# Kernel tuning notes

Measured on AMD Instinct MI355X. Metric: run time of the kernel, lower is better.

## Reference

```python
import jax, jax.numpy as jnp
import numpy as np

TEMPERATURE = 0.1
NORM_EPS = 1e-12          # F.normalize default eps
SMALL_VAL = float(np.finfo(np.float32).tiny)  # pytorch-metric-learning small_val(float32)
NEG_INF = float(np.finfo(np.float32).min)     # c_f.neg_inf for masked logsumexp


def setup_inputs() -> dict:
    key = jax.random.key(0)
    k1, k2 = jax.random.split(key)
    N, D = 8192, 128
    emb = jax.random.normal(k1, (N, D), dtype=jnp.float32)
    labels = jax.random.randint(k2, (N,), 0, 1000, dtype=jnp.int64)
    return {"emb": emb, "labels": labels}


def reference(emb, labels):
    N = emb.shape[0]
    # F.normalize(emb, dim=1): x / max(||x||, eps)
    norms = jnp.linalg.norm(emb, axis=1, keepdims=True)
    x = emb / jnp.maximum(norms, NORM_EPS)

    # cosine similarity matrix [N, N], scaled by temperature
    mat = jnp.matmul(x, x.T) / TEMPERATURE

    same = labels[:, None] == labels[None, :]
    diag = jnp.eye(N, dtype=bool)
    pos_mask = same & ~diag          # same label, i != j
    keep_mask = ~diag                # pos + neg (all off-diagonal)

    # numerical stability: subtract detached row max (over full row, incl. diagonal)
    mat_max = jax.lax.stop_gradient(jnp.max(mat, axis=1, keepdims=True))
    mat = mat - mat_max

    # masked logsumexp over off-diagonal entries
    masked = jnp.where(keep_mask, mat, NEG_INF)
    denom = jax.nn.logsumexp(masked, axis=1, keepdims=True)  # [N, 1]

    log_prob = mat - denom
    pos_f = pos_mask.astype(mat.dtype)
    mean_log_prob_pos = jnp.sum(pos_f * log_prob, axis=1) / (
        jnp.sum(pos_f, axis=1) + SMALL_VAL
    )
    losses = -mean_log_prob_pos  # per-element losses
    # SumReducer: sum over elements
    return jnp.sum(losses)
```

## Files before the change

### kernel.cpp

```cpp
#include <hip/hip_runtime.h>
#include <hip/hip_bf16.h>


typedef __bf16 bf16_t;
typedef __bf16 bf16x2 __attribute__((ext_vector_type(2)));
typedef __bf16 bf16x8 __attribute__((ext_vector_type(8)));
typedef float f32x16 __attribute__((ext_vector_type(16)));

#define NN 8192
#define DIM 128
#define NCLASS 1024
#define MAIN_BLOCKS 2080
#define SMALL_VAL 1.17549435e-38f
#define L2E10 14.4269504089f
#define LN2 0.69314718056f


__global__ __launch_bounds__(256) void normalize_kernel(const float* __restrict__ emb,
                                                        bf16_t* __restrict__ xsw,
                                                        bf16_t* __restrict__ xrow,
                                                        float* __restrict__ se_acc,
                                                        float* __restrict__ out) {
    int row  = blockIdx.x * 4 + (threadIdx.x >> 6);
    int lane = threadIdx.x & 63;
    float2 v = ((const float2*)emb)[row * 64 + lane];
    float ss = v.x * v.x + v.y * v.y;
#pragma unroll
    for (int m = 1; m < 64; m <<= 1) ss += __shfl_xor(ss, m, 64);
    float inv = 1.0f / fmaxf(sqrtf(ss), 1e-12f);
    bf16x2 o; o.x = (bf16_t)(v.x * inv); o.y = (bf16_t)(v.y * inv);
    int f = lane >> 3, hh = (lane >> 2) & 1, j = (lane & 3) << 1;
    *(bf16x2*)(xsw + ((size_t)(row >> 5) * 4096) + f * 512 + hh * 256 + (row & 31) * 8 + j) = o;
    *(bf16x2*)(xrow + (size_t)row * DIM + 2 * lane) = o;
    if (threadIdx.x < 4) se_acc[blockIdx.x * 4 + threadIdx.x] = 0.f;
    if (blockIdx.x == 0 && threadIdx.x == 0) *out = 0.f;
}

__global__ __launch_bounds__(256) void csum_kernel(const bf16_t* __restrict__ xrow,
                                                   const int* __restrict__ labels,
                                                   float* __restrict__ csum,
                                                   int* __restrict__ hist) {
    __shared__ float cs[DIM];
    __shared__ int cw[4];
    int cls = blockIdx.x;
    int wv = threadIdx.x >> 6, lane = threadIdx.x & 63;
    if (threadIdx.x < DIM) cs[threadIdx.x] = 0.f;
    __syncthreads();
    float s0 = 0.f, s1 = 0.f;
    int cnt = 0;
    const int4* lab4 = (const int4*)(labels + wv * 2048);
    for (int it = 0; it < 8; ++it) {
        int4 l = lab4[it * 64 + lane];
        int base = wv * 2048 + it * 256;
#pragma unroll
        for (int cmp = 0; cmp < 4; ++cmp) {
            int li = (cmp == 0) ? l.x : (cmp == 1) ? l.y : (cmp == 2) ? l.z : l.w;
            unsigned long long m = __ballot(li == cls);
            cnt += (int)__popcll(m);
            while (m) {
                int bb = __builtin_ctzll(m);
                m &= m - 1;
                int row = base + 4 * bb + cmp;
                bf16x2 xv = *(const bf16x2*)(xrow + (size_t)row * DIM + 2 * lane);
                s0 += (float)xv.x; s1 += (float)xv.y;
            }
        }
    }
    atomicAdd(&cs[2 * lane], s0);
    atomicAdd(&cs[2 * lane + 1], s1);
    if (lane == 0) cw[wv] = cnt;
    __syncthreads();
    if (threadIdx.x < DIM) csum[(size_t)cls * DIM + threadIdx.x] = cs[threadIdx.x];
    if (threadIdx.x == 0) hist[cls] = cw[0] + cw[1] + cw[2] + cw[3];
}

__global__ __launch_bounds__(256, 4) void supcon_main(const bf16_t* __restrict__ xsw,
                                                      float* __restrict__ se_acc) {
    __shared__ float cols[128];
    if (threadIdx.x < 128) cols[threadIdx.x] = 0.f;
    __syncthreads();

    int b = blockIdx.x;
    int cq = (int)((sqrtf(8.f * (float)b + 1.f) - 1.f) * 0.5f);
    while ((cq + 1) * (cq + 2) / 2 <= b) ++cq;
    while (cq * (cq + 1) / 2 > b) --cq;
    int g = b - cq * (cq + 1) / 2;

    int wv = threadIdx.x >> 6, lane = threadIdx.x & 63;
    int I = 4 * g + wv;
    int c = lane & 31, h = lane >> 5;
    int laneoff = h * 256 + c * 8;

    const bf16_t* abase = xsw + (size_t)I * 4096 + laneoff;
    bf16x8 a[8];
#pragma unroll
    for (int f = 0; f < 8; ++f) a[f] = *(const bf16x8*)(abase + f * 512);

    const bf16_t* bbase = xsw + (size_t)cq * 4 * 4096 + laneoff;

    float se[16];
#pragma unroll
    for (int r = 0; r < 16; ++r) se[r] = 0.f;
    float colacc[4] = {0.f, 0.f, 0.f, 0.f};

#pragma unroll
    for (int t = 0; t < 4; ++t) {
        const bf16_t* bb = bbase + (size_t)t * 4096;
        bf16x8 bfr[8];
#pragma unroll
        for (int f = 0; f < 8; ++f) bfr[f] = *(const bf16x8*)(bb + f * 512);
        f32x16 acc;
#pragma unroll
        for (int r = 0; r < 16; ++r) acc[r] = 0.f;
#pragma unroll
        for (int f = 0; f < 8; ++f)
            acc = __builtin_amdgcn_mfma_f32_32x32x16_bf16(a[f], bfr[f], acc, 0, 0, 0);
        int ct = cq * 4 + t;
        if (ct >= I) {
            float c0 = 0.f, c1 = 0.f, c2 = 0.f, c3 = 0.f;
#pragma unroll
            for (int r = 0; r < 16; ++r) {
                float e = __builtin_amdgcn_exp2f(fmaf(acc[r], L2E10, -L2E10));
                se[r] += e;
                if ((r & 3) == 0) c0 += e; else if ((r & 3) == 1) c1 += e;
                else if ((r & 3) == 2) c2 += e; else c3 += e;
            }
            if (ct > I) colacc[t] = (c0 + c1) + (c2 + c3);
        }
    }

#pragma unroll
    for (int r = 0; r < 16; ++r) {
        float vv = se[r];
#pragma unroll
        for (int m = 1; m < 32; m <<= 1) vv += __shfl_xor(vv, m, 64);
        se[r] = vv;
    }
    if (c == 0) {
        int rowbase = I * 32 + 4 * h;
#pragma unroll
        for (int r = 0; r < 16; ++r)
            atomicAdd(&se_acc[rowbase + (r & 3) + 8 * (r >> 2)], se[r]);
    }

#pragma unroll
    for (int t = 0; t < 4; ++t) {
        float v = colacc[t] + __shfl_xor(colacc[t], 32, 64);
        if (h == 0) atomicAdd(&cols[t * 32 + c], v);
    }
    __syncthreads();
    if (threadIdx.x < 128)
        atomicAdd(&se_acc[cq * 128 + threadIdx.x], cols[threadIdx.x]);
}

__global__ __launch_bounds__(256) void finalize_kernel(const bf16_t* __restrict__ xrow,
                                                       const float* __restrict__ se_acc,
                                                       const float* __restrict__ csum,
                                                       const int* __restrict__ hist,
                                                       const int* __restrict__ labels,
                                                       float* __restrict__ out) {
    __shared__ float part[4];
    int wv = threadIdx.x >> 6, lane = threadIdx.x & 63;
    int wid = blockIdx.x * 4 + wv;
    float lsum = 0.f;
    for (int k = 0; k < 8; ++k) {
        int row = wid * 8 + k;
        int lab = labels[row];
        bf16x2 xv = *(const bf16x2*)(xrow + (size_t)row * DIM + 2 * lane);
        float2 cs = *(const float2*)(csum + (size_t)lab * DIM + 2 * lane);
        float x0 = (float)xv.x, x1 = (float)xv.y;
        float sd = fmaf(x0, x0, x1 * x1);
        float cd = fmaf(x0, cs.x, x1 * cs.y);
#pragma unroll
        for (int m = 1; m < 64; m <<= 1) {
            sd += __shfl_xor(sd, m, 64);
            cd += __shfl_xor(cd, m, 64);
        }
        if (lane == 0) {
            float diag = __builtin_amdgcn_exp2f(fmaf(sd, L2E10, -L2E10));
            float sev  = fmaxf(se_acc[row] - diag, 1e-30f);
            float lse  = fmaf(log2f(sev), LN2, 10.f);
            float cnt  = (float)(hist[lab] - 1);
            float ps   = 10.f * (cd - sd);
            lsum += (cnt * lse - ps) / (cnt + SMALL_VAL);
        }
    }
    if (lane == 0) part[wv] = lsum;
    __syncthreads();
    if (threadIdx.x == 0) atomicAdd(out, part[0] + part[1] + part[2] + part[3]);
}

extern "C" void kernel_launch(void* const* d_in, const int* in_sizes, int n_in,
                              void* d_out, int out_size, void* d_ws, size_t ws_size,
                              hipStream_t stream) {
    const float* emb  = (const float*)d_in[0];
    const int* labels = (const int*)d_in[1];

    char* ws = (char*)d_ws;
    bf16_t* xsw  = (bf16_t*)ws;
    bf16_t* xrow = (bf16_t*)(ws + (size_t)NN * DIM * 2);
    float* csum  = (float*)(ws + 2 * (size_t)NN * DIM * 2);
    int*   hist  = (int*)((char*)csum + (size_t)NCLASS * DIM * 4);
    float* se    = (float*)((char*)hist + NCLASS * 4);

    normalize_kernel<<<NN / 4, 256, 0, stream>>>(emb, xsw, xrow, se, (float*)d_out);
    csum_kernel<<<NCLASS, 256, 0, stream>>>(xrow, labels, csum, hist);
    supcon_main<<<MAIN_BLOCKS, 256, 0, stream>>>(xsw, se);
    finalize_kernel<<<NN / 32, 256, 0, stream>>>(xrow, se, csum, hist, labels, (float*)d_out);
}
```

Before: 109.0 us.

## Fuse normalization into per-class sum kernel and stage B tiles in LDS

New measurement: 99.11 us. 9.1% less time.

```diff
diff --git a/kernel.cpp b/kernel.cpp
--- a/kernel.cpp
+++ b/kernel.cpp
@@ -9,46 +9,38 @@
 
 #define NN 8192
 #define DIM 128
-#define NCLASS 1024
 #define MAIN_BLOCKS 2080
 #define SMALL_VAL 1.17549435e-38f
 #define L2E10 14.4269504089f
 #define LN2 0.69314718056f
 
-
-__global__ __launch_bounds__(256) void normalize_kernel(const float* __restrict__ emb,
-                                                        bf16_t* __restrict__ xsw,
-                                                        bf16_t* __restrict__ xrow,
-                                                        float* __restrict__ se_acc,
-                                                        float* __restrict__ out) {
-    int row  = blockIdx.x * 4 + (threadIdx.x >> 6);
-    int lane = threadIdx.x & 63;
-    float2 v = ((const float2*)emb)[row * 64 + lane];
-    float ss = v.x * v.x + v.y * v.y;
-#pragma unroll
-    for (int m = 1; m < 64; m <<= 1) ss += __shfl_xor(ss, m, 64);
-    float inv = 1.0f / fmaxf(sqrtf(ss), 1e-12f);
-    bf16x2 o; o.x = (bf16_t)(v.x * inv); o.y = (bf16_t)(v.y * inv);
+__device__ inline size_t swz(int row, int lane) {
     int f = lane >> 3, hh = (lane >> 2) & 1, j = (lane & 3) << 1;
-    *(bf16x2*)(xsw + ((size_t)(row >> 5) * 4096) + f * 512 + hh * 256 + (row & 31) * 8 + j) = o;
-    *(bf16x2*)(xrow + (size_t)row * DIM + 2 * lane) = o;
-    if (threadIdx.x < 4) se_acc[blockIdx.x * 4 + threadIdx.x] = 0.f;
-    if (blockIdx.x == 0 && threadIdx.x == 0) *out = 0.f;
-}
-
-__global__ __launch_bounds__(256) void csum_kernel(const bf16_t* __restrict__ xrow,
-                                                   const int* __restrict__ labels,
-                                                   float* __restrict__ csum,
-                                                   int* __restrict__ hist) {
+    return ((size_t)(row >> 5) * 4096) + f * 512 + hh * 256 + (row & 31) * 8 + j;
+}
+
+__global__ __launch_bounds__(256) void norm_csum(const float* __restrict__ emb,
+                                                 const int* __restrict__ labels,
+                                                 bf16_t* __restrict__ xsw,
+                                                 float* __restrict__ cd_arr,
+                                                 float* __restrict__ sd_arr,
+                                                 float* __restrict__ cm1_arr,
+                                                 float* __restrict__ se_acc,
+                                                 float* __restrict__ out) {
     __shared__ float cs[DIM];
-    __shared__ int cw[4];
+    __shared__ int rowlist[96];
+    __shared__ int nrows;
     int cls = blockIdx.x;
     int wv = threadIdx.x >> 6, lane = threadIdx.x & 63;
     if (threadIdx.x < DIM) cs[threadIdx.x] = 0.f;
-    __syncthreads();
+    if (threadIdx.x == 0) nrows = 0;
+    if (threadIdx.x < 8) se_acc[cls * 8 + threadIdx.x] = 0.f;
+    if (cls == 0 && threadIdx.x == 0) *out = 0.f;
+    __syncthreads();
+
     float s0 = 0.f, s1 = 0.f;
-    int cnt = 0;
     const int4* lab4 = (const int4*)(labels + wv * 2048);
+#pragma unroll
     for (int it = 0; it < 8; ++it) {
         int4 l = lab4[it * 64 + lane];
         int base = wv * 2048 + it * 256;
@@ -56,29 +48,51 @@
         for (int cmp = 0; cmp < 4; ++cmp) {
             int li = (cmp == 0) ? l.x : (cmp == 1) ? l.y : (cmp == 2) ? l.z : l.w;
             unsigned long long m = __ballot(li == cls);
-            cnt += (int)__popcll(m);
             while (m) {
                 int bb = __builtin_ctzll(m);
                 m &= m - 1;
                 int row = base + 4 * bb + cmp;
-                bf16x2 xv = *(const bf16x2*)(xrow + (size_t)row * DIM + 2 * lane);
-                s0 += (float)xv.x; s1 += (float)xv.y;
+                float2 v = ((const float2*)emb)[row * 64 + lane];
+                float ss = fmaf(v.x, v.x, v.y * v.y);
+#pragma unroll
+                for (int mm = 1; mm < 64; mm <<= 1) ss += __shfl_xor(ss, mm, 64);
+                float inv = 1.0f / fmaxf(sqrtf(ss), 1e-12f);
+                bf16x2 o; o.x = (bf16_t)(v.x * inv); o.y = (bf16_t)(v.y * inv);
+                *(bf16x2*)(xsw + swz(row, lane)) = o;
+                s0 += (float)o.x; s1 += (float)o.y;
+                if (lane == 0) {
+                    int idx = atomicAdd(&nrows, 1);
+                    if (idx < 96) rowlist[idx] = row;
+                }
             }
         }
     }
     atomicAdd(&cs[2 * lane], s0);
     atomicAdd(&cs[2 * lane + 1], s1);
-    if (lane == 0) cw[wv] = cnt;
-    __syncthreads();
-    if (threadIdx.x < DIM) csum[(size_t)cls * DIM + threadIdx.x] = cs[threadIdx.x];
-    if (threadIdx.x == 0) hist[cls] = cw[0] + cw[1] + cw[2] + cw[3];
+    __syncthreads();
+    int n = nrows;
+    for (int k = wv; k < n; k += 4) {
+        int row = rowlist[k];
+        bf16x2 xv = *(const bf16x2*)(xsw + swz(row, lane));
+        float x0 = (float)xv.x, x1 = (float)xv.y;
+        float cdp = fmaf(x0, cs[2 * lane], x1 * cs[2 * lane + 1]);
+        float sdp = fmaf(x0, x0, x1 * x1);
+#pragma unroll
+        for (int mm = 1; mm < 64; mm <<= 1) {
+            cdp += __shfl_xor(cdp, mm, 64);
+            sdp += __shfl_xor(sdp, mm, 64);
+        }
+        if (lane == 0) {
+            cd_arr[row] = cdp; sd_arr[row] = sdp; cm1_arr[row] = (float)(n - 1);
+        }
+    }
 }
 
 __global__ __launch_bounds__(256, 4) void supcon_main(const bf16_t* __restrict__ xsw,
                                                       float* __restrict__ se_acc) {
+    __shared__ bf16_t bst[4 * 4096];
     __shared__ float cols[128];
     if (threadIdx.x < 128) cols[threadIdx.x] = 0.f;
-    __syncthreads();
 
     int b = blockIdx.x;
     int cq = (int)((sqrtf(8.f * (float)b + 1.f) - 1.f) * 0.5f);
@@ -96,7 +110,14 @@
 #pragma unroll
     for (int f = 0; f < 8; ++f) a[f] = *(const bf16x8*)(abase + f * 512);
 
-    const bf16_t* bbase = xsw + (size_t)cq * 4 * 4096 + laneoff;
+    {
+        const uint4* gsrc = (const uint4*)(xsw + (size_t)cq * 4 * 4096);
+        uint4* ldst = (uint4*)bst;
+#pragma unroll
+        for (int i = 0; i < 8; ++i)
+            ldst[i * 256 + threadIdx.x] = gsrc[i * 256 + threadIdx.x];
+    }
+    __syncthreads();
 
     float se[16];
 #pragma unroll
@@ -105,10 +126,10 @@
 
 #pragma unroll
     for (int t = 0; t < 4; ++t) {
-        const bf16_t* bb = bbase + (size_t)t * 4096;
+        const bf16_t* bt = bst + t * 4096 + laneoff;
         bf16x8 bfr[8];
 #pragma unroll
-        for (int f = 0; f < 8; ++f) bfr[f] = *(const bf16x8*)(bb + f * 512);
+        for (int f = 0; f < 8; ++f) bfr[f] = *(const bf16x8*)(bt + f * 512);
         f32x16 acc;
 #pragma unroll
         for (int r = 0; r < 16; ++r) acc[r] = 0.f;
@@ -153,39 +174,22 @@
         atomicAdd(&se_acc[cq * 128 + threadIdx.x], cols[threadIdx.x]);
 }
 
-__global__ __launch_bounds__(256) void finalize_kernel(const bf16_t* __restrict__ xrow,
-                                                       const float* __restrict__ se_acc,
-                                                       const float* __restrict__ csum,
-                                                       const int* __restrict__ hist,
-                                                       const int* __restrict__ labels,
+__global__ __launch_bounds__(256) void finalize_kernel(const float* __restrict__ se_acc,
+                                                       const float* __restrict__ cd_arr,
+                                                       const float* __restrict__ sd_arr,
+                                                       const float* __restrict__ cm1_arr,
                                                        float* __restrict__ out) {
     __shared__ float part[4];
-    int wv = threadIdx.x >> 6, lane = threadIdx.x & 63;
-    int wid = blockIdx.x * 4 + wv;
-    float lsum = 0.f;
-    for (int k = 0; k < 8; ++k) {
-        int row = wid * 8 + k;
-        int lab = labels[row];
-        bf16x2 xv = *(const bf16x2*)(xrow + (size_t)row * DIM + 2 * lane);
-        float2 cs = *(const float2*)(csum + (size_t)lab * DIM + 2 * lane);
-        float x0 = (float)xv.x, x1 = (float)xv.y;
-        float sd = fmaf(x0, x0, x1 * x1);
-        float cd = fmaf(x0, cs.x, x1 * cs.y);
-#pragma unroll
-        for (int m = 1; m < 64; m <<= 1) {
-            sd += __shfl_xor(sd, m, 64);
-            cd += __shfl_xor(cd, m, 64);
-        }
-        if (lane == 0) {
-            float diag = __builtin_amdgcn_exp2f(fmaf(sd, L2E10, -L2E10));
-            float sev  = fmaxf(se_acc[row] - diag, 1e-30f);
-            float lse  = fmaf(log2f(sev), LN2, 10.f);
-            float cnt  = (float)(hist[lab] - 1);
-            float ps   = 10.f * (cd - sd);
-            lsum += (cnt * lse - ps) / (cnt + SMALL_VAL);
-        }
-    }
-    if (lane == 0) part[wv] = lsum;
+    int i = blockIdx.x * 256 + threadIdx.x;
+    float sd = sd_arr[i], cd = cd_arr[i], cm1 = cm1_arr[i];
+    float diag = __builtin_amdgcn_exp2f(fmaf(sd, L2E10, -L2E10));
+    float sev  = fmaxf(se_acc[i] - diag, 1e-30f);
+    float lse  = fmaf(__builtin_amdgcn_logf(sev), LN2, 10.f);
+    float loss = (cm1 * lse - 10.f * (cd - sd)) / (cm1 + SMALL_VAL);
+#pragma unroll
+    for (int m = 1; m < 64; m <<= 1) loss += __shfl_xor(loss, m, 64);
+    int wv = threadIdx.x >> 6;
+    if ((threadIdx.x & 63) == 0) part[wv] = loss;
     __syncthreads();
     if (threadIdx.x == 0) atomicAdd(out, part[0] + part[1] + part[2] + part[3]);
 }
@@ -197,14 +201,13 @@
     const int* labels = (const int*)d_in[1];
 
     char* ws = (char*)d_ws;
-    bf16_t* xsw  = (bf16_t*)ws;
-    bf16_t* xrow = (bf16_t*)(ws + (size_t)NN * DIM * 2);
-    float* csum  = (float*)(ws + 2 * (size_t)NN * DIM * 2);
-    int*   hist  = (int*)((char*)csum + (size_t)NCLASS * DIM * 4);
-    float* se    = (float*)((char*)hist + NCLASS * 4);
-
-    normalize_kernel<<<NN / 4, 256, 0, stream>>>(emb, xsw, xrow, se, (float*)d_out);
-    csum_kernel<<<NCLASS, 256, 0, stream>>>(xrow, labels, csum, hist);
+    bf16_t* xsw = (bf16_t*)ws;
+    float* se   = (float*)(ws + (size_t)NN * DIM * 2);
+    float* cd   = se + NN;
+    float* sd   = cd + NN;
+    float* cm1  = sd + NN;
+
+    norm_csum<<<1024, 256, 0, stream>>>(emb, labels, xsw, cd, sd, cm1, se, (float*)d_out);
     supcon_main<<<MAIN_BLOCKS, 256, 0, stream>>>(xsw, se);
-    finalize_kernel<<<NN / 32, 256, 0, stream>>>(xrow, se, csum, hist, labels, (float*)d_out);
-}
+    finalize_kernel<<<NN / 256, 256, 0, stream>>>(se, cd, sd, cm1, (float*)d_out);
+}
```
